# Performance work log

Measured on AMD Instinct MI355X. Metric: run time of the kernel, lower is better.

The kernel has to match this reference:

```python
import jax, jax.numpy as jnp
import numpy as np
from jax import lax

N, H, W, C = 4, 256, 256, 128
COUT = 128
BS_IN, BS_OUT, BSTR = 18, 16, 16  # gather block, conv-out block, block stride
N_ACTIVE = 512


def setup_inputs() -> dict:
    key = jax.random.key(0)
    ks = jax.random.split(key, 8)
    x = jax.random.normal(ks[0], (N, H, W, C), dtype=jnp.float32)
    w = jax.random.normal(ks[1], (3, 3, C, COUT), dtype=jnp.float32) * 0.05  # HWIO
    b = jax.random.normal(ks[2], (COUT,), dtype=jnp.float32) * 0.05
    gamma = jax.random.uniform(ks[3], (COUT,), dtype=jnp.float32, minval=0.5, maxval=1.5)
    beta = jax.random.normal(ks[4], (COUT,), dtype=jnp.float32) * 0.1
    mean = jax.random.normal(ks[5], (COUT,), dtype=jnp.float32) * 0.1
    var = jax.random.uniform(ks[6], (COUT,), dtype=jnp.float32, minval=0.5, maxval=1.5)
    # unique active block ids over the N x (H/16) x (W/16) grid -> disjoint scatter targets
    n_blocks = N * (H // BSTR) * (W // BSTR)
    active = jax.random.permutation(ks[7], n_blocks)[:N_ACTIVE].astype(jnp.int32)
    return {"x": x, "w": w, "b": b, "gamma": gamma, "beta": beta,
            "mean": mean, "var": var, "active": active}


def reference(x, w, b, gamma, beta, mean, var, active):
    n_, h_, w_, c_ = x.shape
    nby, nbx = h_ // BSTR, w_ // BSTR
    bn = active // (nby * nbx)
    rem = active % (nby * nbx)
    by = rem // nbx
    bx = rem % nbx

    # --- sparse_gather: overlapping BS_IN x BS_IN input blocks (zero-pad edges) ---
    pad = BS_IN - BS_OUT
    xp = jnp.pad(x, ((0, 0), (0, pad), (0, pad), (0, 0)))
    Hp, Wp = h_ + pad, w_ + pad
    d_in = jnp.arange(BS_IN, dtype=jnp.int32)
    hs = by[:, None] * BSTR + d_in[None, :]            # [Nb, 18]
    ws = bx[:, None] * BSTR + d_in[None, :]            # [Nb, 18]
    gidx = bn[:, None, None] * (Hp * Wp) + hs[:, :, None] * Wp + ws[:, None, :]
    p = xp.reshape(-1, c_)[gidx]                       # [Nb, 18, 18, C]

    # --- dense conv + BN(eval, eps=1e-3) + ReLU on gathered blocks ---
    q = lax.conv_general_dilated(p, w, window_strides=(1, 1), padding='VALID',
                                 dimension_numbers=('NHWC', 'HWIO', 'NHWC'))
    q = q + b
    q = (q - mean) * (gamma * lax.rsqrt(var + 1e-3)) + beta
    q = jax.nn.relu(q)                                 # [Nb, 16, 16, COUT]

    # --- sparse_scatter: write disjoint BS_OUT blocks back into a copy of x ---
    d_out = jnp.arange(BS_OUT, dtype=jnp.int32)
    hso = by[:, None] * BSTR + d_out[None, :]
    wso = bx[:, None] * BSTR + d_out[None, :]
    sidx = bn[:, None, None] * (h_ * w_) + hso[:, :, None] * w_ + wso[:, None, :]
    y = x.reshape(-1, c_).at[sidx.reshape(-1)].set(q.reshape(-1, q.shape[-1]))
    return y.reshape(n_, h_, w_, c_)
```

## Files before the change

### kernel.cpp

```cpp
#include <hip/hip_runtime.h>
#include <hip/hip_bf16.h>

#define H_ 256
#define W_ 256
#define C_ 128
#define NBPOS 1024
#define NACT 512

typedef __bf16 bf16x8 __attribute__((ext_vector_type(8)));
typedef float f32x4 __attribute__((ext_vector_type(4)));

#define SCALE_OFF 294912
#define SHIFT_OFF 295424
#define INACT_OFF 295936

__global__ void prep_kernel(const float* __restrict__ w, const float* __restrict__ b,
                            const float* __restrict__ gamma, const float* __restrict__ beta,
                            const float* __restrict__ mean, const float* __restrict__ var,
                            const int* __restrict__ active,
                            __bf16* __restrict__ wprep, float* __restrict__ scale,
                            float* __restrict__ shift, int* __restrict__ inact) {
  int blk = blockIdx.x, tid = threadIdx.x;
  if (blk < 576) {
    int o = blk * 256 + tid;
    int j = o & 7, cout = (o >> 3) & 127, k8 = (o >> 10) & 15, tap = o >> 14;
    wprep[o] = (__bf16)w[((size_t)tap * 128 + k8 * 8 + j) * 128 + cout];
    return;
  }
  __shared__ unsigned mask[32];
  __shared__ int cnt;
  if (tid < 32) mask[tid] = 0u;
  if (tid == 0) cnt = 0;
  __syncthreads();
  for (int i = tid; i < NACT; i += 256) {
    int a = active[i];
    atomicOr(&mask[a >> 5], 1u << (a & 31));
  }
  if (tid < 128) {
    float s = gamma[tid] * rsqrtf(var[tid] + 1e-3f);
    scale[tid] = s;
    shift[tid] = (b[tid] - mean[tid]) * s + beta[tid];
  }
  __syncthreads();
  for (int p = tid; p < NBPOS; p += 256) {
    if (!((mask[p >> 5] >> (p & 31)) & 1u)) {
      int q = atomicAdd(&cnt, 1);
      inact[q] = p;
    }
  }
}

__global__ __launch_bounds__(256, 4) void main_kernel(
    const float* __restrict__ x, const __bf16* __restrict__ wprep,
    const float* __restrict__ scale, const float* __restrict__ shift,
    const int* __restrict__ active, const int* __restrict__ inact,
    float* __restrict__ y) {
  __shared__ unsigned char ldsA[180 * 128];

  const int idx = blockIdx.x;
  const int tid = threadIdx.x;

  if (idx % 3 == 2) {
    const int cid = inact[idx / 3];
    const int cn = cid >> 8, cy = (cid >> 4) & 15, cx = cid & 15;
    const size_t base4 = ((((size_t)cn * H_ + cy * 16) * W_ + cx * 16) * C_) >> 2;
    const f32x4* __restrict__ xs = (const f32x4*)x;
    f32x4* __restrict__ ys = (f32x4*)y;
#pragma unroll 4
    for (int i = 0; i < 32; ++i) {
      int lin = (i << 8) + tid;
      int row = lin >> 9, rem = lin & 511;
      size_t idx4 = base4 + (size_t)row * (W_ * C_ / 4) + rem;
      f32x4 v = xs[idx4];
      __builtin_nontemporal_store(v, &ys[idx4]);
    }
    return;
  }

  const int j = (idx / 3) * 2 + (idx % 3);
  const int lane = tid & 63;
  const int wid = tid >> 6;
  const int aid = active[j >> 1];
  const int mh = j & 1;
  const int bn = aid >> 8, by = (aid >> 4) & 15, bx = aid & 15;
  const int h0 = by * 16, w0 = bx * 16;
  const int hm = h0 + mh * 8;
  const float* xb = x + (size_t)bn * (H_ * W_ * C_);

  f32x4 acc[2][8];
  f32x4 zero = {0.f, 0.f, 0.f, 0.f};
#pragma unroll
  for (int i = 0; i < 2; ++i)
#pragma unroll
    for (int jj = 0; jj < 8; ++jj) acc[i][jj] = zero;

  const bf16x8* __restrict__ wq = (const bf16x8*)wprep;
  const int koff = (lane >> 4) * 16;
  const int sbl = ((lane >> 4) << 7) + (lane & 15);

  auto stage = [&](int half) {
    for (int u = tid; u < 180 * 8; u += 256) {
      int s = u >> 3, c8 = u & 7;
      int pr = s / 18, col = s - pr * 18;
      int hs = hm + pr, wsp = w0 + col;
      float4 f0 = make_float4(0.f, 0.f, 0.f, 0.f), f1 = f0;
      if (hs < H_ && wsp < W_) {
        const float* p = xb + (size_t)(hs * W_ + wsp) * C_ + half * 64 + c8 * 8;
        f0 = *(const float4*)p;
        f1 = *(const float4*)(p + 4);
      }
      bf16x8 v;
      v[0] = (__bf16)f0.x; v[1] = (__bf16)f0.y; v[2] = (__bf16)f0.z; v[3] = (__bf16)f0.w;
      v[4] = (__bf16)f1.x; v[5] = (__bf16)f1.y; v[6] = (__bf16)f1.z; v[7] = (__bf16)f1.w;
      int lin = s * 128 + c8 * 16;
      *(bf16x8*)(&ldsA[lin ^ ((s & 7) << 4)]) = v;
    }
  };

  for (int half = 0; half < 2; ++half) {
    if (half) __syncthreads();
    stage(half);
    __syncthreads();

#pragma unroll 2
    for (int ks = 0; ks < 18; ++ks) {
      int tap = ks >> 1, kch = ks & 1;
      int dyv = tap / 3, dxv = tap - dyv * 3;
      int tile = tap * 4 + half * 2 + kch;

      bf16x8 a[2];
#pragma unroll
      for (int mi = 0; mi < 2; ++mi) {
        int srow = (wid * 2 + mi + dyv) * 18 + dxv + (lane & 15);
        int lin = srow * 128 + kch * 64 + koff;
        a[mi] = *(const bf16x8*)(&ldsA[lin ^ ((srow & 7) << 4)]);
      }
      bf16x8 bfr[8];
      int sb = tile * 512 + sbl;
#pragma unroll
      for (int nb = 0; nb < 8; ++nb)
        bfr[nb] = wq[sb + nb * 16];
#pragma unroll
      for (int mi = 0; mi < 2; ++mi)
#pragma unroll
        for (int nb = 0; nb < 8; ++nb)
          acc[mi][nb] = __builtin_amdgcn_mfma_f32_16x16x32_bf16(a[mi], bfr[nb], acc[mi][nb], 0, 0, 0);
    }
  }

  const int colc = lane & 15;
  float sc[8], sh[8];
#pragma unroll
  for (int nb = 0; nb < 8; ++nb) {
    sc[nb] = scale[nb * 16 + colc];
    sh[nb] = shift[nb * 16 + colc];
  }
  float* yb = y + (((size_t)bn * H_ + hm) * W_ + w0) * C_;
#pragma unroll
  for (int mi = 0; mi < 2; ++mi) {
    int oy = wid * 2 + mi;
#pragma unroll
    for (int r = 0; r < 4; ++r) {
      int ox = (lane >> 4) * 4 + r;
      float* yr = yb + ((size_t)oy * W_ + ox) * C_;
#pragma unroll
      for (int nb = 0; nb < 8; ++nb) {
        float v = acc[mi][nb][r] * sc[nb] + sh[nb];
        __builtin_nontemporal_store(fmaxf(v, 0.f), &yr[nb * 16 + colc]);
      }
    }
  }
}

extern "C" void kernel_launch(void* const* d_in, const int* in_sizes, int n_in,
                              void* d_out, int out_size, void* d_ws, size_t ws_size,
                              hipStream_t stream) {
  const float* x     = (const float*)d_in[0];
  const float* w     = (const float*)d_in[1];
  const float* b     = (const float*)d_in[2];
  const float* gamma = (const float*)d_in[3];
  const float* beta  = (const float*)d_in[4];
  const float* mean  = (const float*)d_in[5];
  const float* var   = (const float*)d_in[6];
  const int*   act   = (const int*)d_in[7];
  float* y = (float*)d_out;
  char* ws = (char*)d_ws;
  __bf16* wprep = (__bf16*)ws;
  float* scale = (float*)(ws + SCALE_OFF);
  float* shift = (float*)(ws + SHIFT_OFF);
  int* inact = (int*)(ws + INACT_OFF);

  prep_kernel<<<dim3(577), dim3(256), 0, stream>>>(w, b, gamma, beta, mean, var, act,
                                                   wprep, scale, shift, inact);
  main_kernel<<<dim3(1536), dim3(256), 0, stream>>>(x, wprep, scale, shift, act, inact, y);
}
```

Measured before the change: 79.29 us.

## Split conv blocks into quarter-row tiles with output-channel halves per wave

Each active 16x16 block is now processed by four workgroups of 4 output rows instead of two workgroups of 8 rows. Within a workgroup the four waves form a 2x2 grid over rows and output-channel halves, so each wave holds 8 accumulators instead of 16. The LDS tile shrinks to 6x18 pixels, launch bounds rise to 5 and the grid doubles, and the copy blocks are split into half-blocks to match. The aim is more occupancy and parallelism, at the cost of more redundant halo gathering (6 rows staged per 4 output rows) and more A-fragment LDS reads per MFMA.

```diff
diff --git a/kernel.cpp b/kernel.cpp
--- a/kernel.cpp
+++ b/kernel.cpp
@@ -50,29 +50,30 @@
   }
 }
 
-__global__ __launch_bounds__(256, 4) void main_kernel(
+__global__ __launch_bounds__(256, 5) void main_kernel(
     const float* __restrict__ x, const __bf16* __restrict__ wprep,
     const float* __restrict__ scale, const float* __restrict__ shift,
     const int* __restrict__ active, const int* __restrict__ inact,
     float* __restrict__ y) {
-  __shared__ unsigned char ldsA[180 * 128];
+  __shared__ unsigned char ldsA[108 * 128];
 
   const int idx = blockIdx.x;
   const int tid = threadIdx.x;
 
   if (idx % 3 == 2) {
-    const int cid = inact[idx / 3];
+    const int k = idx / 3;
+    const int cid = inact[k >> 1];
+    const int ch = k & 1;
     const int cn = cid >> 8, cy = (cid >> 4) & 15, cx = cid & 15;
-    const size_t base4 = ((((size_t)cn * H_ + cy * 16) * W_ + cx * 16) * C_) >> 2;
+    const size_t base4 = ((((size_t)cn * H_ + cy * 16 + ch * 8) * W_ + cx * 16) * C_) >> 2;
     const f32x4* __restrict__ xs = (const f32x4*)x;
     f32x4* __restrict__ ys = (f32x4*)y;
 #pragma unroll 4
-    for (int i = 0; i < 32; ++i) {
+    for (int i = 0; i < 16; ++i) {
       int lin = (i << 8) + tid;
-      int row = lin >> 9, rem = lin & 511;
-      size_t idx4 = base4 + (size_t)row * (W_ * C_ / 4) + rem;
-      f32x4 v = xs[idx4];
-      __builtin_nontemporal_store(v, &ys[idx4]);
+      size_t i4 = base4 + (size_t)(lin >> 9) * (W_ * C_ / 4) + (lin & 511);
+      f32x4 v = xs[i4];
+      __builtin_nontemporal_store(v, &ys[i4]);
     }
     return;
   }
@@ -80,29 +81,30 @@
   const int j = (idx / 3) * 2 + (idx % 3);
   const int lane = tid & 63;
   const int wid = tid >> 6;
-  const int aid = active[j >> 1];
-  const int mh = j & 1;
+  const int wm = wid >> 1, wn = wid & 1;
+  const int aid = active[j >> 2];
+  const int q = j & 3;
   const int bn = aid >> 8, by = (aid >> 4) & 15, bx = aid & 15;
   const int h0 = by * 16, w0 = bx * 16;
-  const int hm = h0 + mh * 8;
+  const int hq = h0 + q * 4;
   const float* xb = x + (size_t)bn * (H_ * W_ * C_);
 
-  f32x4 acc[2][8];
+  f32x4 acc[2][4];
   f32x4 zero = {0.f, 0.f, 0.f, 0.f};
 #pragma unroll
   for (int i = 0; i < 2; ++i)
 #pragma unroll
-    for (int jj = 0; jj < 8; ++jj) acc[i][jj] = zero;
+    for (int jj = 0; jj < 4; ++jj) acc[i][jj] = zero;
 
   const bf16x8* __restrict__ wq = (const bf16x8*)wprep;
   const int koff = (lane >> 4) * 16;
-  const int sbl = ((lane >> 4) << 7) + (lane & 15);
+  const int sbl = ((lane >> 4) << 7) + (wn << 6) + (lane & 15);
 
   auto stage = [&](int half) {
-    for (int u = tid; u < 180 * 8; u += 256) {
+    for (int u = tid; u < 108 * 8; u += 256) {
       int s = u >> 3, c8 = u & 7;
       int pr = s / 18, col = s - pr * 18;
-      int hs = hm + pr, wsp = w0 + col;
+      int hs = hq + pr, wsp = w0 + col;
       float4 f0 = make_float4(0.f, 0.f, 0.f, 0.f), f1 = f0;
       if (hs < H_ && wsp < W_) {
         const float* p = xb + (size_t)(hs * W_ + wsp) * C_ + half * 64 + c8 * 8;
@@ -122,7 +124,7 @@
     stage(half);
     __syncthreads();
 
-#pragma unroll 2
+#pragma unroll 3
     for (int ks = 0; ks < 18; ++ks) {
       int tap = ks >> 1, kch = ks & 1;
       int dyv = tap / 3, dxv = tap - dyv * 3;
@@ -131,42 +133,42 @@
       bf16x8 a[2];
 #pragma unroll
       for (int mi = 0; mi < 2; ++mi) {
-        int srow = (wid * 2 + mi + dyv) * 18 + dxv + (lane & 15);
+        int srow = (wm * 2 + mi + dyv) * 18 + dxv + (lane & 15);
         int lin = srow * 128 + kch * 64 + koff;
         a[mi] = *(const bf16x8*)(&ldsA[lin ^ ((srow & 7) << 4)]);
       }
-      bf16x8 bfr[8];
+      bf16x8 bfr[4];
       int sb = tile * 512 + sbl;
 #pragma unroll
-      for (int nb = 0; nb < 8; ++nb)
+      for (int nb = 0; nb < 4; ++nb)
         bfr[nb] = wq[sb + nb * 16];
 #pragma unroll
       for (int mi = 0; mi < 2; ++mi)
 #pragma unroll
-        for (int nb = 0; nb < 8; ++nb)
+        for (int nb = 0; nb < 4; ++nb)
           acc[mi][nb] = __builtin_amdgcn_mfma_f32_16x16x32_bf16(a[mi], bfr[nb], acc[mi][nb], 0, 0, 0);
     }
   }
 
   const int colc = lane & 15;
-  float sc[8], sh[8];
+  float sc[4], sh[4];
 #pragma unroll
-  for (int nb = 0; nb < 8; ++nb) {
-    sc[nb] = scale[nb * 16 + colc];
-    sh[nb] = shift[nb * 16 + colc];
+  for (int nb = 0; nb < 4; ++nb) {
+    sc[nb] = scale[wn * 64 + nb * 16 + colc];
+    sh[nb] = shift[wn * 64 + nb * 16 + colc];
   }
-  float* yb = y + (((size_t)bn * H_ + hm) * W_ + w0) * C_;
+  float* yb = y + (((size_t)bn * H_ + hq) * W_ + w0) * C_;
 #pragma unroll
   for (int mi = 0; mi < 2; ++mi) {
-    int oy = wid * 2 + mi;
+    int oy = wm * 2 + mi;
 #pragma unroll
     for (int r = 0; r < 4; ++r) {
       int ox = (lane >> 4) * 4 + r;
       float* yr = yb + ((size_t)oy * W_ + ox) * C_;
 #pragma unroll
-      for (int nb = 0; nb < 8; ++nb) {
+      for (int nb = 0; nb < 4; ++nb) {
         float v = acc[mi][nb][r] * sc[nb] + sh[nb];
-        __builtin_nontemporal_store(fmaxf(v, 0.f), &yr[nb * 16 + colc]);
+        __builtin_nontemporal_store(fmaxf(v, 0.f), &yr[wn * 64 + nb * 16 + colc]);
       }
     }
   }
@@ -192,5 +194,5 @@
 
   prep_kernel<<<dim3(577), dim3(256), 0, stream>>>(w, b, gamma, beta, mean, var, act,
                                                    wprep, scale, shift, inact);
-  main_kernel<<<dim3(1536), dim3(256), 0, stream>>>(x, wprep, scale, shift, act, inact, y);
+  main_kernel<<<dim3(3072), dim3(256), 0, stream>>>(x, wprep, scale, shift, act, inact, y);
 }
```

After: 82.20 us. +3.7%, slower.
